# Kernel tuning notes

Measured on AMD Instinct MI355X. Metric: run time of the kernel, lower is better.

Reference implementation:

```python
import jax, jax.numpy as jnp
import numpy as np

H, K, TP = 15, 15, 8          # h bits, k=c*h candidates per bit, tp coordinates
NLOC = 2 ** H                  # 32768 code space
NNODES, BATCH, DMAX = 100000, 128, 64
EPS, GAMMA, ALPHA, POS_RATIO = 0.1, 2.0, 1.0, 1.0
NCAND = H * K + 1              # 226 connection candidates


def setup_inputs() -> dict:
    key = jax.random.key(0)
    k1, k2, k3, k4, k5, k6, k7 = jax.random.split(key, 7)
    degree = jax.random.randint(k1, (NNODES,), 1, DMAX + 1, dtype=jnp.int32)
    locations = jax.random.randint(k2, (NNODES, TP), 0, NLOC, dtype=jnp.int32)
    sta_ind = jax.random.permutation(k3, NNODES)[:BATCH].astype(jnp.int32)  # unique batch nodes
    lg = degree[sta_ind]
    mask = jnp.arange(DMAX, dtype=jnp.int32)[None, :] < lg[:, None]         # [B,D] valid neighbors
    pos_ind = jnp.where(mask, jax.random.randint(k4, (BATCH, DMAX), 0, NNODES, dtype=jnp.int32), -1)
    neg_ind = jnp.where(mask, jax.random.randint(k5, (BATCH, DMAX), 0, NNODES, dtype=jnp.int32), -1)
    upper = (jnp.int32(1) << jnp.arange(H, dtype=jnp.int32))                # 2^j per flipped bit
    random_masks = jax.random.randint(k6, (BATCH, H, K, TP), 0, NLOC, dtype=jnp.int32) % upper[None, :, None, None]
    perm = jax.random.permutation(k7, NCAND).astype(jnp.int32)              # candidate shuffle
    xs = jnp.arange(NLOC)
    lut = jnp.where(xs == 0, 0.0,
                    jnp.floor(jnp.log2(jnp.maximum(xs, 1).astype(jnp.float32))) + 1.0).astype(jnp.float32)
    return {"lut": lut, "sta_ind": sta_ind, "locations": locations, "degree": degree,
            "pos_ind": pos_ind, "neg_ind": neg_ind, "random_masks": random_masks, "perm": perm}


def _p(lut_dis, degree, sta_ind, ig2):
    # p(dis, ig1, ig2) from the torch module; ig2 may contain -1 (torch wraps to last row)
    deg1 = degree[sta_ind][:, None]                                   # [B,1]
    ig2w = jnp.where(ig2 < 0, ig2 + NNODES, ig2)
    deg2 = degree[ig2w]                                               # [B,D]
    log_ap = jnp.log(((deg1 + 1) * (deg2 + 1)).astype(jnp.float32))   # [B,D]
    aa = (lut_dis + EPS) / log_ap[:, :, None, None]
    return 1.0 / (1.0 + aa ** GAMMA / ALPHA)


def reference(lut, sta_ind, locations, degree, pos_ind, neg_ind, random_masks, perm):
    mask = pos_ind != -1                                              # [B,D]
    lg = mask.sum(axis=1).astype(jnp.float32)                         # == degree[sta_ind]
    sta_loc = locations[sta_ind]                                      # [B,tp]
    pos_loc = jnp.where(mask[:, :, None], locations[jnp.where(mask, pos_ind, 0)], -1)  # [B,D,tp]
    neg_loc = jnp.where(mask[:, :, None], locations[jnp.where(mask, neg_ind, 0)], -1)

    # connection(): flip each of H bits, XOR with K random low-bit masks, plus the original point
    flip = (jnp.int32(1) << jnp.arange(H, dtype=jnp.int32))[None, :, None]
    flipped = sta_loc[:, None, :] ^ flip                              # [B,H,tp]
    cand = (flipped[:, :, None, :] ^ random_masks).reshape(sta_loc.shape[0], H * K, TP)
    cnc_loc = jnp.concatenate([cand, sta_loc[:, None, :]], axis=1)[:, perm, :]  # [B,C,tp]

    m1 = mask[:, :, None]                                             # [B,D,1]
    m2 = mask[:, :, None, None]                                       # [B,D,1,1]

    def dist(xor, m):
        return jnp.where(m, lut[jnp.where(m, xor, 0)], -1.0)

    dis_sta_pos = dist(sta_loc[:, None, :] ^ pos_loc, m1)             # [B,D,tp]
    dis_sta_posum = dis_sta_pos.sum(axis=-1)                          # [B,D]
    dis_sta_neg = dist(sta_loc[:, None, :] ^ neg_loc, m1)
    dis_sta_negum = dis_sta_neg.sum(axis=-1)

    dis_pos_cnc = dist(cnc_loc[:, None, :, :] ^ pos_loc[:, :, None, :], m2)  # [B,D,C,tp]
    dis_neg_cnc = dist(cnc_loc[:, None, :, :] ^ neg_loc[:, :, None, :], m2)

    dis_new_pos = jnp.where(m2, (dis_pos_cnc - dis_sta_pos[:, :, None, :]
                                 + dis_sta_posum[:, :, None, None]) / TP, 0.0)
    dis_new_neg = jnp.where(m2, (dis_neg_cnc - dis_sta_neg[:, :, None, :]
                                 + dis_sta_negum[:, :, None, None]) / TP, 1000.0)

    pos_loss = -jnp.sum(jnp.log(_p(dis_new_pos, degree, sta_ind, pos_ind)), axis=1) / lg[:, None, None]
    neg_loss = -jnp.sum(jnp.log(1.0 + EPS - _p(dis_new_neg, degree, sta_ind, neg_ind)), axis=1) / lg[:, None, None]
    total_loss = POS_RATIO * pos_loss + neg_loss                      # [B,C,tp]

    index = jnp.argmin(total_loss, axis=1)                            # [B,tp] best candidate per coord
    sel_loc = jnp.take_along_axis(cnc_loc, index[:, None, :], axis=1)[:, 0, :]  # [B,tp]
    new_locations = locations.at[sta_ind].set(sel_loc)                # scatter update

    def gather_sel(x):
        return jnp.take_along_axis(x, index[:, None, :], axis=1)[:, 0, :]

    tl = jnp.mean(gather_sel(total_loss))
    pl = jnp.mean(gather_sel(pos_loss))
    nl = jnp.mean(gather_sel(neg_loss))
    return (jnp.stack([tl, pl, nl]), new_locations)
```

## Files before the change

### kernel.cpp

```cpp
#include <hip/hip_runtime.h>
#include <math.h>

constexpr int TPC    = 8;
constexpr int NNODES = 100000;
constexpr int BATCH  = 128;
constexpr int DMAX   = 64;
constexpr int Hc     = 15;
constexpr int Kc     = 15;
constexpr int NCAND  = Hc * Kc + 1;


__device__ __forceinline__ int bl_of(int x, const int* __restrict__ powlut) {
    const int idx = 32 - __clz(x);
    return ((x & (x - 1)) == 0) ? powlut[idx] : idx;
}

__global__ void copy_kernel(const int* __restrict__ loc, float* __restrict__ out) {
    int i = blockIdx.x * blockDim.x + threadIdx.x;
    const int total = NNODES * TPC;
    for (int idx = i; idx < total; idx += gridDim.x * blockDim.x)
        out[3 + idx] = (float)loc[idx];
}

__launch_bounds__(256)
__global__ void main_kernel(const float* __restrict__ lut,
                            const int* __restrict__ sta_ind,
                            const int* __restrict__ locations,
                            const int* __restrict__ degree,
                            const int* __restrict__ pos_ind,
                            const int* __restrict__ neg_ind,
                            const int* __restrict__ rmasks,
                            const int* __restrict__ perm,
                            float* __restrict__ ws,
                            float* __restrict__ out) {
    __shared__ float Tp[64][32];
    __shared__ float Tn[64][32];
    __shared__ int   ploc[64], nloc[64];
    __shared__ int   Sarr[2][64];
    __shared__ float Lsq[2][64];
    __shared__ float logLsq[64];
    __shared__ int   dsarr[2][64];
    __shared__ int   varr[2][64];
    __shared__ int   sh_sta[8];
    __shared__ int   powlut[16];
    __shared__ float lg_sh;
    __shared__ float cpos[256], cneg[256];
    __shared__ int   cval_sh[256];
    __shared__ float wmin[4];
    __shared__ int   widx[4];

    const int b   = blockIdx.x >> 3;
    const int t   = blockIdx.x & 7;
    const int tid = threadIdx.x;
    const int sta = sta_ind[b];

    if (tid < 8) sh_sta[tid] = locations[sta * 8 + tid];
    if (tid >= 16 && tid < 32) {
        const int i = tid - 16;
        powlut[i] = (i == 0) ? (int)lut[0] : (int)lut[1 << (i - 1)];
    }
    __syncthreads();

    if (tid < 128) {
        const int which = tid >> 6;
        const int d     = tid & 63;
        const int* ind  = which ? neg_ind : pos_ind;
        const int pi    = ind[b * DMAX + d];
        const int valid = (pi >= 0) ? 1 : 0;
        const int piw   = valid ? pi : pi + NNODES;
        const int deg1  = degree[sta];
        const int deg2  = degree[piw];
        const float L   = logf((float)((deg1 + 1) * (deg2 + 1)));
        int Si = 0, dsi = 0, lc = -1;
        if (valid) {
            #pragma unroll
            for (int tt = 0; tt < 8; ++tt) {
                const int l  = locations[pi * 8 + tt];
                const int x  = sh_sta[tt] ^ l;
                const int bl = bl_of(x, powlut);
                Si += bl;
                if (tt == t) { dsi = bl; lc = l; }
            }
        }
        const float lsq = L * L;
        Sarr[which][d]  = Si;
        Lsq[which][d]   = lsq;
        if (which == 0) logLsq[d] = logf(lsq);
        dsarr[which][d] = dsi;
        varr[which][d]  = valid;
        if (which == 0) ploc[d] = lc; else nloc[d] = lc;
        if (which == 0) {
            unsigned long long m = __ballot(valid);
            if (tid == 0) lg_sh = (float)__popcll(m);
        }
    }
    __syncthreads();

    for (int e = tid; e < 4096; e += 256) {
        const int which = e >> 11;
        const int rem   = e & 2047;
        const int d     = rem >> 5;
        const int slot  = rem & 31;
        const int g     = (slot < 16) ? slot : powlut[slot - 16];
        const float lsq = Lsq[which][d];
        float x;
        if (varr[which][d])
            x = (float)(g - dsarr[which][d] + Sarr[which][d]) * 0.125f;
        else
            x = which ? 1000.0f : 0.0f;
        const float y  = x + 0.1f;
        const float s  = lsq + y * y;
        const float ls = logf(s);
        float term;
        if (which) term = ls - logf(0.1f * lsq + 1.1f * y * y);
        else       term = ls - logLsq[d];
        if (which) Tn[d][slot] = term; else Tp[d][slot] = term;
    }
    __syncthreads();

    const int c = tid;
    float v = __builtin_inff();
    float plc = 0.0f, nlc = 0.0f;
    int cval = 0;
    if (c < NCAND) {
        const int q  = perm[c];
        const int st = sh_sta[t];
        if (q < NCAND - 1) {
            const int h = q / Kc, k = q % Kc;
            cval = st ^ (1 << h) ^ rmasks[((b * Hc + h) * Kc + k) * 8 + t];
        } else {
            cval = st;
        }
        float ps = 0.0f, ns = 0.0f;
        #pragma unroll 8
        for (int d = 0; d < 64; ++d) {
            const int xp = (cval ^ ploc[d]) & 0x7FFF;
            const int ip = (32 - __clz(xp)) + (((xp & (xp - 1)) == 0) ? 16 : 0);
            ps += Tp[d][ip];
            const int xn = (cval ^ nloc[d]) & 0x7FFF;
            const int in_ = (32 - __clz(xn)) + (((xn & (xn - 1)) == 0) ? 16 : 0);
            ns += Tn[d][in_];
        }
        const float lg = lg_sh;
        plc = ps / lg;
        nlc = ns / lg;
        v   = plc + nlc;
    }
    cpos[tid]    = plc;
    cneg[tid]    = nlc;
    cval_sh[tid] = cval;

    int idx = tid;
    #pragma unroll
    for (int m = 32; m >= 1; m >>= 1) {
        const float ov = __shfl_xor(v, m, 64);
        const int   oi = __shfl_xor(idx, m, 64);
        if (ov < v || (ov == v && oi < idx)) { v = ov; idx = oi; }
    }
    if ((tid & 63) == 0) { wmin[tid >> 6] = v; widx[tid >> 6] = idx; }
    __syncthreads();

    if (tid == 0) {
        float bv = wmin[0];
        int   bi = widx[0];
        #pragma unroll
        for (int w = 1; w < 4; ++w) {
            const float vv = wmin[w];
            const int   ii = widx[w];
            if (vv < bv || (vv == bv && ii < bi)) { bv = vv; bi = ii; }
        }
        ws[blockIdx.x]          = bv;
        ws[1024 + blockIdx.x]   = cpos[bi];
        ws[2048 + blockIdx.x]   = cneg[bi];
        out[3 + sta * 8 + t]    = (float)cval_sh[bi];
    }
}

__launch_bounds__(256)
__global__ void reduce_kernel(const float* __restrict__ ws, float* __restrict__ out) {
    const int tid = threadIdx.x;
    __shared__ float wsum[3][4];
    #pragma unroll
    for (int a = 0; a < 3; ++a) {
        float s = 0.0f;
        #pragma unroll
        for (int j = 0; j < 4; ++j) s += ws[a * 1024 + j * 256 + tid];
        #pragma unroll
        for (int m = 32; m >= 1; m >>= 1) s += __shfl_xor(s, m, 64);
        if ((tid & 63) == 0) wsum[a][tid >> 6] = s;
    }
    __syncthreads();
    if (tid < 3)
        out[tid] = (wsum[tid][0] + wsum[tid][1] + wsum[tid][2] + wsum[tid][3])
                   * (1.0f / 1024.0f);
}

extern "C" void kernel_launch(void* const* d_in, const int* in_sizes, int n_in,
                              void* d_out, int out_size, void* d_ws, size_t ws_size,
                              hipStream_t stream) {
    const float* lut     = (const float*)d_in[0];
    const int* sta_ind   = (const int*)d_in[1];
    const int* locations = (const int*)d_in[2];
    const int* degree    = (const int*)d_in[3];
    const int* pos_ind   = (const int*)d_in[4];
    const int* neg_ind   = (const int*)d_in[5];
    const int* rmasks    = (const int*)d_in[6];
    const int* perm      = (const int*)d_in[7];
    float* out = (float*)d_out;
    float* ws  = (float*)d_ws;

    hipLaunchKernelGGL(copy_kernel, dim3(1024), dim3(256), 0, stream, locations, out);
    hipLaunchKernelGGL(main_kernel, dim3(BATCH * TPC), dim3(256), 0, stream,
                       lut, sta_ind, locations, degree, pos_ind, neg_ind, rmasks, perm, ws, out);
    hipLaunchKernelGGL(reduce_kernel, dim3(1), dim3(256), 0, stream, ws, out);
}
```

Baseline: 100.3 us.

## Fuse location copy into main kernel and defer selected-location scatter to finish kernel

Removes the separate copy kernel by having each main-kernel block copy a strided slice of the locations array into the output. Because copies and scattered updates can now race, the chosen candidate values go to workspace and the final reduce kernel scatters them into the output. Neighbor locations are now read as two int4 vector loads, and the 0x7FFF masks in the inner loop are dropped. This saves one kernel launch and its serialization, at the cost of extra work per main block and an added serial scatter in the single-block finish kernel.

```diff
diff --git a/kernel.cpp b/kernel.cpp
--- a/kernel.cpp
+++ b/kernel.cpp
@@ -8,19 +8,8 @@
 constexpr int Hc     = 15;
 constexpr int Kc     = 15;
 constexpr int NCAND  = Hc * Kc + 1;
-
-
-__device__ __forceinline__ int bl_of(int x, const int* __restrict__ powlut) {
-    const int idx = 32 - __clz(x);
-    return ((x & (x - 1)) == 0) ? powlut[idx] : idx;
-}
-
-__global__ void copy_kernel(const int* __restrict__ loc, float* __restrict__ out) {
-    int i = blockIdx.x * blockDim.x + threadIdx.x;
-    const int total = NNODES * TPC;
-    for (int idx = i; idx < total; idx += gridDim.x * blockDim.x)
-        out[3 + idx] = (float)loc[idx];
-}
+constexpr int NLOCF  = NNODES * TPC;
+
 
 __launch_bounds__(256)
 __global__ void main_kernel(const float* __restrict__ lut,
@@ -31,7 +20,8 @@
                             const int* __restrict__ neg_ind,
                             const int* __restrict__ rmasks,
                             const int* __restrict__ perm,
-                            float* __restrict__ ws,
+                            float* __restrict__ wsf,
+                            int*   __restrict__ wsi,
                             float* __restrict__ out) {
     __shared__ float Tp[64][32];
     __shared__ float Tn[64][32];
@@ -49,10 +39,14 @@
     __shared__ float wmin[4];
     __shared__ int   widx[4];
 
-    const int b   = blockIdx.x >> 3;
-    const int t   = blockIdx.x & 7;
+    const int bid = blockIdx.x;
+    const int b   = bid >> 3;
+    const int t   = bid & 7;
     const int tid = threadIdx.x;
     const int sta = sta_ind[b];
+
+    for (int idx = bid * 256 + tid; idx < NLOCF; idx += 1024 * 256)
+        out[3 + idx] = (float)locations[idx];
 
     if (tid < 8) sh_sta[tid] = locations[sta * 8 + tid];
     if (tid >= 16 && tid < 32) {
@@ -71,15 +65,18 @@
         const int deg1  = degree[sta];
         const int deg2  = degree[piw];
         const float L   = logf((float)((deg1 + 1) * (deg2 + 1)));
-        int Si = 0, dsi = 0, lc = -1;
+        int Si = 0, dsi = 0, lc = 0;
         if (valid) {
+            const int4* lp = reinterpret_cast<const int4*>(locations + pi * 8);
+            const int4 va = lp[0], vb = lp[1];
+            const int l0[8] = {va.x, va.y, va.z, va.w, vb.x, vb.y, vb.z, vb.w};
             #pragma unroll
             for (int tt = 0; tt < 8; ++tt) {
-                const int l  = locations[pi * 8 + tt];
-                const int x  = sh_sta[tt] ^ l;
-                const int bl = bl_of(x, powlut);
+                const int x   = sh_sta[tt] ^ l0[tt];
+                const int idx = 32 - __clz(x);
+                const int bl  = ((x & (x - 1)) == 0) ? powlut[idx] : idx;
                 Si += bl;
-                if (tt == t) { dsi = bl; lc = l; }
+                if (tt == t) { dsi = bl; lc = l0[tt]; }
             }
         }
         const float lsq = L * L;
@@ -134,12 +131,12 @@
         float ps = 0.0f, ns = 0.0f;
         #pragma unroll 8
         for (int d = 0; d < 64; ++d) {
-            const int xp = (cval ^ ploc[d]) & 0x7FFF;
-            const int ip = (32 - __clz(xp)) + (((xp & (xp - 1)) == 0) ? 16 : 0);
-            ps += Tp[d][ip];
-            const int xn = (cval ^ nloc[d]) & 0x7FFF;
-            const int in_ = (32 - __clz(xn)) + (((xn & (xn - 1)) == 0) ? 16 : 0);
-            ns += Tn[d][in_];
+            const int xp = cval ^ ploc[d];
+            const int bp = 32 - __clz(xp);
+            ps += Tp[d][((xp & (xp - 1)) == 0) ? bp + 16 : bp];
+            const int xn = cval ^ nloc[d];
+            const int bn = 32 - __clz(xn);
+            ns += Tn[d][((xn & (xn - 1)) == 0) ? bn + 16 : bn];
         }
         const float lg = lg_sh;
         plc = ps / lg;
@@ -169,25 +166,34 @@
             const int   ii = widx[w];
             if (vv < bv || (vv == bv && ii < bi)) { bv = vv; bi = ii; }
         }
-        ws[blockIdx.x]          = bv;
-        ws[1024 + blockIdx.x]   = cpos[bi];
-        ws[2048 + blockIdx.x]   = cneg[bi];
-        out[3 + sta * 8 + t]    = (float)cval_sh[bi];
+        wsf[bid]        = bv;
+        wsf[1024 + bid] = cpos[bi];
+        wsf[2048 + bid] = cneg[bi];
+        wsi[bid]        = cval_sh[bi];
     }
 }
 
 __launch_bounds__(256)
-__global__ void reduce_kernel(const float* __restrict__ ws, float* __restrict__ out) {
+__global__ void finish_kernel(const int* __restrict__ sta_ind,
+                              const float* __restrict__ wsf,
+                              const int* __restrict__ wsi,
+                              float* __restrict__ out) {
     const int tid = threadIdx.x;
     __shared__ float wsum[3][4];
     #pragma unroll
     for (int a = 0; a < 3; ++a) {
         float s = 0.0f;
         #pragma unroll
-        for (int j = 0; j < 4; ++j) s += ws[a * 1024 + j * 256 + tid];
+        for (int j = 0; j < 4; ++j) s += wsf[a * 1024 + j * 256 + tid];
         #pragma unroll
         for (int m = 32; m >= 1; m >>= 1) s += __shfl_xor(s, m, 64);
         if ((tid & 63) == 0) wsum[a][tid >> 6] = s;
+    }
+    #pragma unroll
+    for (int j = 0; j < 4; ++j) {
+        const int i = j * 256 + tid;
+        const int b = i >> 3, t = i & 7;
+        out[3 + sta_ind[b] * 8 + t] = (float)wsi[i];
     }
     __syncthreads();
     if (tid < 3)
@@ -207,10 +213,12 @@
     const int* rmasks    = (const int*)d_in[6];
     const int* perm      = (const int*)d_in[7];
     float* out = (float*)d_out;
-    float* ws  = (float*)d_ws;
-
-    hipLaunchKernelGGL(copy_kernel, dim3(1024), dim3(256), 0, stream, locations, out);
+    float* wsf = (float*)d_ws;
+    int*   wsi = (int*)d_ws + 3072;
+
     hipLaunchKernelGGL(main_kernel, dim3(BATCH * TPC), dim3(256), 0, stream,
-                       lut, sta_ind, locations, degree, pos_ind, neg_ind, rmasks, perm, ws, out);
-    hipLaunchKernelGGL(reduce_kernel, dim3(1), dim3(256), 0, stream, ws, out);
+                       lut, sta_ind, locations, degree, pos_ind, neg_ind, rmasks, perm,
+                       wsf, wsi, out);
+    hipLaunchKernelGGL(finish_kernel, dim3(1), dim3(256), 0, stream,
+                       sta_ind, wsf, wsi, out);
 }
```

Result: faster. 95.67 us (-4.6%).
